# Kernel tuning notes

Measured on AMD Instinct MI355X. Metric: run time of the kernel, lower is better.

The kernel has to match this reference:

```python
import jax, jax.numpy as jnp
import numpy as np

N, E, D, H = 50000, 400000, 64, 2  # nodes, edges, model_dim, heads


def setup_inputs() -> dict:
    key = jax.random.key(0)
    ks = jax.random.split(key, 11)
    lim = 1.0 / np.sqrt(D)        # torch Linear default init bound (fan_in = D)
    lim_o = 1.0 / np.sqrt(H * D)  # O has fan_in = H*D under merge='cat'
    u = lambda k, shape, l: jax.random.uniform(k, shape, jnp.float32, -l, l)
    return {
        "node_feature": jax.random.normal(ks[0], (N, D), jnp.float32),
        "Wk": u(ks[1], (H, D, D), lim), "bk": u(ks[2], (H, D), lim),
        "Wq": u(ks[3], (H, D, D), lim), "bq": u(ks[4], (H, D), lim),
        "Wv": u(ks[5], (H, D, D), lim), "bv": u(ks[6], (H, D), lim),
        "Wo": u(ks[7], (D, H * D), lim_o), "bo": u(ks[8], (D,), lim_o),
        "src": jax.random.randint(ks[9], (E,), 0, N, jnp.int32),
        "dst": jax.random.randint(ks[10], (E,), 0, N, jnp.int32),
    }


def reference(node_feature, Wk, bk, Wq, bq, Wv, bv, Wo, bo, src, dst):
    # message_func: per-edge gather + per-head K/Q/V linears (torch Linear: x @ W.T + b)
    src_nf = node_feature[src]                               # [E, D]
    dst_nf = node_feature[dst]                               # [E, D]
    k = jnp.einsum('ed,hfd->ehf', src_nf, Wk) + bk           # [E, H, D]
    q = jnp.einsum('ed,hfd->ehf', dst_nf, Wq) + bq           # [E, H, D]
    v = jnp.einsum('ed,hfd->ehf', src_nf, Wv) + bv           # [E, H, D]
    score = jnp.sum(k * q, axis=-1)                          # [E, H]

    # reduce_func: mailbox softmax over incoming edges per dst node (segment softmax)
    m = jax.ops.segment_max(score, dst, num_segments=N)      # [N, H]
    m = jnp.where(jnp.isfinite(m), m, jnp.zeros_like(m))     # nodes with no in-edges
    es = jnp.exp(score - m[dst])                             # [E, H]
    denom = jax.ops.segment_sum(es, dst, num_segments=N)     # [N, H]
    w = es / denom[dst]                                      # [E, H] attention weights
    wv = jax.ops.segment_sum(w[..., None] * v, dst, num_segments=N)  # [N, H, D]

    # apply_nodes: merge='cat' over heads, then O linear; weight = mean over heads
    out_nf = jnp.einsum('nf,of->no', wv.reshape(N, H * D), Wo) + bo  # [N, D]
    edge_weight = w.mean(axis=-1)                            # [E] (per-edge, mean over heads)
    return out_nf, edge_weight
```

## Files before the change

kernel.cpp:

```cpp
#include <hip/hip_runtime.h>
#include <hip/hip_bf16.h>
#include <cstdint>


#define BCAP 32

using short8 = __attribute__((ext_vector_type(8))) short;
using f32x4 = __attribute__((ext_vector_type(4))) float;

__device__ __forceinline__ unsigned short f2bf(float f) {
  __hip_bfloat16 h = __float2bfloat16(f);
  return *reinterpret_cast<unsigned short*>(&h);
}
__device__ __forceinline__ void bf8(const uint4 u, float* f) {
  union { unsigned int i; float v; } a;
  a.i = u.x << 16; f[0] = a.v;  a.i = u.x & 0xffff0000u; f[1] = a.v;
  a.i = u.y << 16; f[2] = a.v;  a.i = u.y & 0xffff0000u; f[3] = a.v;
  a.i = u.z << 16; f[4] = a.v;  a.i = u.z & 0xffff0000u; f[5] = a.v;
  a.i = u.w << 16; f[6] = a.v;  a.i = u.w & 0xffff0000u; f[7] = a.v;
}
__device__ __forceinline__ float dot8(const uint4 a, const uint4 b, float s) {
  float af[8], bfv[8];
  bf8(a, af);
  bf8(b, bfv);
#pragma unroll
  for (int j = 0; j < 8; ++j) s += af[j] * bfv[j];
  return s;
}
__device__ __forceinline__ float gmax16(float v) {
#pragma unroll
  for (int m = 1; m < 16; m <<= 1) v = fmaxf(v, __shfl_xor(v, m, 64));
  return v;
}
__device__ __forceinline__ float gsum16(float v) {
#pragma unroll
  for (int m = 1; m < 16; m <<= 1) v += __shfl_xor(v, m, 64);
  return v;
}

__global__ __launch_bounds__(256) void prep_kernel(
    const float* __restrict__ nf, unsigned short* __restrict__ nfb,
    const float* __restrict__ Wk, const float* __restrict__ Wq,
    const float* __restrict__ Wv, const float* __restrict__ Wo,
    const float* __restrict__ bq, const float* __restrict__ bv,
    const float* __restrict__ bo,
    unsigned short* __restrict__ Mb, unsigned short* __restrict__ Fb,
    float* __restrict__ qb, float* __restrict__ fbias,
    const int* __restrict__ src, const int* __restrict__ dst,
    int* __restrict__ cnt, int2* __restrict__ bucket,
    int nf_f4, int E, int SB, int FB) {
  if (blockIdx.x < SB) {
    for (int idx = blockIdx.x * 256 + threadIdx.x; idx < 16576; idx += SB * 256) {
      if (idx < 8192) {
        const int hf = idx >> 6, j = idx & 63, h = hf >> 6, f = hf & 63;
        const float* wkp = Wk + h * 4096 + f;
        const float* wqp = Wq + h * 4096 + j;
        float s = 0.f;
        for (int i = 0; i < 64; ++i) s += wkp[i * 64] * wqp[i * 64];
        Mb[idx] = f2bf(s);
      } else if (idx < 16384) {
        const int r = idx - 8192;
        const int o = r >> 7, hj = r & 127, h = hj >> 6, j = hj & 63;
        const float* wop = Wo + o * 128 + h * 64;
        const float* wvp = Wv + h * 4096 + j;
        float s = 0.f;
        for (int i = 0; i < 64; ++i) s += wop[i] * wvp[i * 64];
        Fb[r] = f2bf(s);
      } else if (idx < 16512) {
        const int hf = idx - 16384, h = hf >> 6, f = hf & 63;
        const float* wkp = Wk + h * 4096 + f;
        const float* bqp = bq + h * 64;
        float s = 0.f;
        for (int i = 0; i < 64; ++i) s += wkp[i * 64] * bqp[i];
        qb[hf] = s;
      } else if (idx < 16576) {
        const int o = idx - 16512;
        float s = bo[o];
        for (int hi = 0; hi < 128; ++hi) s += Wo[o * 128 + hi] * bv[hi];
        fbias[o] = s;
      }
    }
    return;
  }
  if (blockIdx.x < SB + FB) {
    for (int i = (blockIdx.x - SB) * 256 + threadIdx.x; i < nf_f4; i += FB * 256) {
      const float4 x = ((const float4*)nf)[i];
      uint2 p;
      p.x = (unsigned)f2bf(x.x) | ((unsigned)f2bf(x.y) << 16);
      p.y = (unsigned)f2bf(x.z) | ((unsigned)f2bf(x.w) << 16);
      ((uint2*)nfb)[i] = p;
    }
    return;
  }
  const int CB = gridDim.x - SB - FB;
  for (int e = (blockIdx.x - SB - FB) * 256 + threadIdx.x; e < E; e += CB * 256) {
    const int d = dst[e];
    const int pos = atomicAdd(&cnt[d], 1);
    if (pos < BCAP) bucket[(size_t)d * BCAP + pos] = make_int2(e, src[e]);
  }
}

__global__ __launch_bounds__(256) void qt_kernel(
    const unsigned short* __restrict__ nfb, const unsigned short* __restrict__ Mb,
    const float* __restrict__ qb, unsigned short* __restrict__ Qtb, int N) {
  const int lane = threadIdx.x & 63;
  const int wid = threadIdx.x >> 6;
  const int base = (blockIdx.x * 4 + wid) * 32;
  if (base >= N) return;
  const int col = lane & 15;
  const int kslot = lane >> 4;
  const int k0 = kslot * 8;

  short8 fb[2][2];
#pragma unroll
  for (int t = 0; t < 2; ++t) {
    const int node = min(base + t * 16 + col, N - 1);
    const unsigned short* np = nfb + (size_t)node * 64;
    fb[t][0] = *(const short8*)(np + k0);
    fb[t][1] = *(const short8*)(np + 32 + k0);
  }

#pragma unroll
  for (int t8 = 0; t8 < 8; ++t8) {
    const unsigned short* mp = Mb + (size_t)(t8 * 16 + col) * 64;
    const short8 fa0 = *(const short8*)(mp + k0);
    const short8 fa1 = *(const short8*)(mp + 32 + k0);
    const int wf = t8 * 16 + kslot * 4;
    const float4 bias = *(const float4*)(qb + wf);
#pragma unroll
    for (int t = 0; t < 2; ++t) {
      f32x4 acc = {0.f, 0.f, 0.f, 0.f};
      acc = __builtin_amdgcn_mfma_f32_16x16x32_bf16(fa0, fb[t][0], acc, 0, 0, 0);
      acc = __builtin_amdgcn_mfma_f32_16x16x32_bf16(fa1, fb[t][1], acc, 0, 0, 0);
      const int node = base + t * 16 + col;
      if (node < N) {
        uint2 p;
        p.x = (unsigned)f2bf(acc[0] + bias.x) | ((unsigned)f2bf(acc[1] + bias.y) << 16);
        p.y = (unsigned)f2bf(acc[2] + bias.z) | ((unsigned)f2bf(acc[3] + bias.w) << 16);
        *(uint2*)(Qtb + (size_t)node * 128 + wf) = p;
      }
    }
  }
}

__global__ __launch_bounds__(256) void node_kernel(
    const unsigned short* __restrict__ nfb, const unsigned short* __restrict__ Qtb,
    const int2* __restrict__ bucket, const int* __restrict__ cnt,
    const unsigned short* __restrict__ Fb, const float* __restrict__ fbias,
    const float* __restrict__ bo,
    float* __restrict__ out, float* __restrict__ eout, int N) {
  __shared__ uint4 swv[16][16];

  const int lane = threadIdx.x & 63;
  const int wid = threadIdx.x >> 6;
  const int sl = lane & 15;
  const int g16 = lane & 48;
  const int c8 = sl & 7;
  const int nl = wid * 4 + (lane >> 4);
  const int node = blockIdx.x * 16 + nl;
  const bool valid = node < N;
  const int nodeq = valid ? node : N - 1;
  const int deg = valid ? min(cnt[node], BCAP) : 0;

  int wdeg = deg;
  wdeg = max(wdeg, __shfl_xor(wdeg, 16, 64));
  wdeg = max(wdeg, __shfl_xor(wdeg, 32, 64));
  wdeg = __builtin_amdgcn_readfirstlane(wdeg);

  const uint4 qt = ((const uint4*)(Qtb + (size_t)nodeq * 128))[sl];

  uint4 packed = make_uint4(0u, 0u, 0u, 0u);

  if (wdeg <= 16) {
    int2 es = make_int2(0, 0);
    if (sl < deg) es = bucket[(size_t)nodeq * BCAP + sl];
    const int e_my = es.x;
    const int s_my = (sl < deg) ? es.y : 0;

    int s_i[16];
#pragma unroll
    for (int i = 0; i < 16; ++i) s_i[i] = __shfl(s_my, g16 + i, 64);

    uint4 x_i[16];
#pragma unroll
    for (int i = 0; i < 16; ++i)
      x_i[i] = *(const uint4*)(nfb + (size_t)s_i[i] * 64 + c8 * 8);

    float sc0 = -1e30f, sc1 = -1e30f;
#pragma unroll
    for (int i = 0; i < 16; ++i) {
      float p = dot8(x_i[i], qt, 0.f);
#pragma unroll
      for (int m = 1; m < 8; m <<= 1) p += __shfl_xor(p, m, 64);
      const float other = __shfl_xor(p, 8, 64);
      const float t0 = (sl < 8) ? p : other;
      const float t1 = (sl < 8) ? other : p;
      if (sl == i) { sc0 = t0; sc1 = t1; }
    }
    if (sl >= deg) { sc0 = -1e30f; sc1 = -1e30f; }

    const float m0 = gmax16(sc0);
    const float m1 = gmax16(sc1);
    const float w0 = __expf(sc0 - m0);
    const float w1 = __expf(sc1 - m1);
    const float den0 = gsum16(w0);
    const float den1 = gsum16(w1);
    if (sl < deg) eout[e_my] = 0.5f * (w0 / den0 + w1 / den1);

    float agg[8];
#pragma unroll
    for (int j = 0; j < 8; ++j) agg[j] = 0.f;
#pragma unroll
    for (int i = 0; i < 16; ++i) {
      const float wi0 = __shfl(w0, g16 + i, 64);
      const float wi1 = __shfl(w1, g16 + i, 64);
      float xf[8];
      bf8(x_i[i], xf);
      const float ws = (sl < 8) ? wi0 : wi1;
#pragma unroll
      for (int j = 0; j < 8; ++j) agg[j] += ws * xf[j];
    }
    const float dinv = (deg == 0) ? 0.f : ((sl < 8) ? 1.f / den0 : 1.f / den1);
    unsigned short ob[8];
#pragma unroll
    for (int j = 0; j < 8; ++j) ob[j] = f2bf(agg[j] * dinv);
    packed = *(const uint4*)ob;
  } else {
    float m0 = -1e30f, m1 = -1e30f, den0 = 0.f, den1 = 0.f;
    float agg[8];
#pragma unroll
    for (int j = 0; j < 8; ++j) agg[j] = 0.f;

    for (int c0 = 0; c0 < deg; c0 += 16) {
      const int cn = min(16, deg - c0);
      int s_my = 0;
      if (sl < cn) s_my = bucket[(size_t)nodeq * BCAP + c0 + sl].y;

      int s_i[16];
#pragma unroll
      for (int i = 0; i < 16; ++i) s_i[i] = __shfl(s_my, g16 + i, 64);
      uint4 x_i[16];
#pragma unroll
      for (int i = 0; i < 16; ++i)
        x_i[i] = *(const uint4*)(nfb + (size_t)s_i[i] * 64 + c8 * 8);

      float sc0 = -1e30f, sc1 = -1e30f;
#pragma unroll
      for (int i = 0; i < 16; ++i) {
        float p = dot8(x_i[i], qt, 0.f);
#pragma unroll
        for (int m = 1; m < 8; m <<= 1) p += __shfl_xor(p, m, 64);
        const float other = __shfl_xor(p, 8, 64);
        const float t0 = (sl < 8) ? p : other;
        const float t1 = (sl < 8) ? other : p;
        if (sl == i) { sc0 = t0; sc1 = t1; }
      }
      if (sl >= cn) { sc0 = -1e30f; sc1 = -1e30f; }

      const float cm0 = gmax16(sc0);
      const float cm1 = gmax16(sc1);
      const float nm0 = fmaxf(m0, cm0), nm1 = fmaxf(m1, cm1);
      const float r0 = __expf(m0 - nm0), r1 = __expf(m1 - nm1);
      den0 *= r0; den1 *= r1;
      const float racc = (sl < 8) ? r0 : r1;
#pragma unroll
      for (int j = 0; j < 8; ++j) agg[j] *= racc;
      m0 = nm0; m1 = nm1;

      const float w0 = __expf(sc0 - m0);
      const float w1 = __expf(sc1 - m1);
      den0 += gsum16(w0);
      den1 += gsum16(w1);

#pragma unroll
      for (int i = 0; i < 16; ++i) {
        const float wi0 = __shfl(w0, g16 + i, 64);
        const float wi1 = __shfl(w1, g16 + i, 64);
        float xf[8];
        bf8(x_i[i], xf);
        const float ws = (sl < 8) ? wi0 : wi1;
#pragma unroll
        for (int j = 0; j < 8; ++j) agg[j] += ws * xf[j];
      }
    }

    const float dinv = (deg == 0) ? 0.f : ((sl < 8) ? 1.f / den0 : 1.f / den1);
    unsigned short ob[8];
#pragma unroll
    for (int j = 0; j < 8; ++j) ob[j] = f2bf(agg[j] * dinv);
    packed = *(const uint4*)ob;

    for (int i = 0; i < deg; ++i) {
      const int2 es = bucket[(size_t)nodeq * BCAP + i];
      const uint4 xv = *(const uint4*)(nfb + (size_t)es.y * 64 + c8 * 8);
      float p = dot8(xv, qt, 0.f);
#pragma unroll
      for (int m = 1; m < 8; m <<= 1) p += __shfl_xor(p, m, 64);
      const float other = __shfl_xor(p, 8, 64);
      const float t0 = (sl < 8) ? p : other;
      const float t1 = (sl < 8) ? other : p;
      if (sl == 0)
        eout[es.x] = 0.5f * (__expf(t0 - m0) / den0 + __expf(t1 - m1) / den1);
    }
  }

  swv[nl][sl ^ nl] = packed;
  __syncthreads();

  const int col16 = lane & 15;
  const int hi = lane >> 4;
  short8 fa[4];
#pragma unroll
  for (int c = 0; c < 4; ++c)
    fa[c] = *(const short8*)&swv[col16][(c * 4 + hi) ^ col16];

  const int o = wid * 16 + col16;
  const unsigned short* bp = Fb + (size_t)o * 128;
  f32x4 acco = {0.f, 0.f, 0.f, 0.f};
#pragma unroll
  for (int c = 0; c < 4; ++c) {
    const short8 fbb = *(const short8*)(bp + c * 32 + hi * 8);
    acco = __builtin_amdgcn_mfma_f32_16x16x32_bf16(fa[c], fbb, acco, 0, 0, 0);
  }
  const float fb_o = fbias[o];
  const float bo_o = bo[o];
#pragma unroll
  for (int r = 0; r < 4; ++r) {
    const int nrow = blockIdx.x * 16 + hi * 4 + r;
    if (nrow < N) {
      const float bias = (cnt[nrow] > 0) ? fb_o : bo_o;
      out[(size_t)nrow * 64 + o] = acco[r] + bias;
    }
  }
}

extern "C" void kernel_launch(void* const* d_in, const int* in_sizes, int n_in,
                              void* d_out, int out_size, void* d_ws, size_t ws_size,
                              hipStream_t stream) {
  const float* nf = (const float*)d_in[0];
  const float* Wk = (const float*)d_in[1];
  const float* Wq = (const float*)d_in[3];
  const float* bq = (const float*)d_in[4];
  const float* Wv = (const float*)d_in[5];
  const float* bv = (const float*)d_in[6];
  const float* Wo = (const float*)d_in[7];
  const float* bo = (const float*)d_in[8];
  const int* src = (const int*)d_in[9];
  const int* dst = (const int*)d_in[10];

  const int N = in_sizes[0] / 64;
  const int E = in_sizes[9];

  float* out_nf = (float*)d_out;
  float* eout = (float*)d_out + (size_t)N * 64;

  char* w = (char*)d_ws;
  auto alloc = [&](size_t bytes) -> void* {
    void* p = (void*)w;
    w += (bytes + 255) / 256 * 256;
    return p;
  };
  unsigned short* nfb = (unsigned short*)alloc((size_t)N * 64 * 2);
  unsigned short* Qtb = (unsigned short*)alloc((size_t)N * 128 * 2);
  unsigned short* Mb = (unsigned short*)alloc((size_t)128 * 64 * 2);
  unsigned short* Fb = (unsigned short*)alloc((size_t)64 * 128 * 2);
  float* qb = (float*)alloc(128 * 4);
  float* fbias = (float*)alloc(64 * 4);
  int* cnt = (int*)alloc((size_t)N * 4);
  int2* bucket = (int2*)alloc((size_t)N * BCAP * 8);

  const int SB = 16;
  const int FB = 128;
  const int CB = 256;
  const int nf_f4 = (N * 64) / 4;

  hipMemsetAsync(cnt, 0, (size_t)N * 4, stream);

  prep_kernel<<<SB + FB + CB, 256, 0, stream>>>(
      nf, nfb, Wk, Wq, Wv, Wo, bq, bv, bo, Mb, Fb, qb, fbias, src, dst, cnt,
      bucket, nf_f4, E, SB, FB);
  qt_kernel<<<(N + 127) / 128, 256, 0, stream>>>(nfb, Mb, qb, Qtb, N);
  node_kernel<<<(N + 15) / 16, 256, 0, stream>>>(nfb, Qtb, bucket, cnt, Fb,
                                                 fbias, bo, out_nf, eout, N);
}
```

Measured before the change: 103.9 us.

## Fuse per-node Q-transform MFMA into node kernel via shared memory

Removes the separate qt_kernel and computes each block's 16 nodes' transformed query vectors inside node_kernel with MFMA, storing them in a swizzled shared-memory tile instead of a global Qtb buffer. This eliminates one kernel launch and the global write and read of an N x 128 bf16 intermediate. In exchange it adds a __syncthreads, extra shared memory and a reload of the Mb weights per block, which may lower occupancy slightly.

```diff
diff --git a/kernel.cpp b/kernel.cpp
--- a/kernel.cpp
+++ b/kernel.cpp
@@ -100,64 +100,54 @@
   }
 }
 
-__global__ __launch_bounds__(256) void qt_kernel(
-    const unsigned short* __restrict__ nfb, const unsigned short* __restrict__ Mb,
-    const float* __restrict__ qb, unsigned short* __restrict__ Qtb, int N) {
-  const int lane = threadIdx.x & 63;
-  const int wid = threadIdx.x >> 6;
-  const int base = (blockIdx.x * 4 + wid) * 32;
-  if (base >= N) return;
-  const int col = lane & 15;
-  const int kslot = lane >> 4;
-  const int k0 = kslot * 8;
-
-  short8 fb[2][2];
-#pragma unroll
-  for (int t = 0; t < 2; ++t) {
-    const int node = min(base + t * 16 + col, N - 1);
-    const unsigned short* np = nfb + (size_t)node * 64;
-    fb[t][0] = *(const short8*)(np + k0);
-    fb[t][1] = *(const short8*)(np + 32 + k0);
-  }
-
-#pragma unroll
-  for (int t8 = 0; t8 < 8; ++t8) {
-    const unsigned short* mp = Mb + (size_t)(t8 * 16 + col) * 64;
-    const short8 fa0 = *(const short8*)(mp + k0);
-    const short8 fa1 = *(const short8*)(mp + 32 + k0);
-    const int wf = t8 * 16 + kslot * 4;
-    const float4 bias = *(const float4*)(qb + wf);
-#pragma unroll
-    for (int t = 0; t < 2; ++t) {
-      f32x4 acc = {0.f, 0.f, 0.f, 0.f};
-      acc = __builtin_amdgcn_mfma_f32_16x16x32_bf16(fa0, fb[t][0], acc, 0, 0, 0);
-      acc = __builtin_amdgcn_mfma_f32_16x16x32_bf16(fa1, fb[t][1], acc, 0, 0, 0);
-      const int node = base + t * 16 + col;
-      if (node < N) {
-        uint2 p;
-        p.x = (unsigned)f2bf(acc[0] + bias.x) | ((unsigned)f2bf(acc[1] + bias.y) << 16);
-        p.y = (unsigned)f2bf(acc[2] + bias.z) | ((unsigned)f2bf(acc[3] + bias.w) << 16);
-        *(uint2*)(Qtb + (size_t)node * 128 + wf) = p;
-      }
-    }
-  }
-}
-
 __global__ __launch_bounds__(256) void node_kernel(
-    const unsigned short* __restrict__ nfb, const unsigned short* __restrict__ Qtb,
+    const unsigned short* __restrict__ nfb,
+    const unsigned short* __restrict__ Mb, const float* __restrict__ qb,
     const int2* __restrict__ bucket, const int* __restrict__ cnt,
     const unsigned short* __restrict__ Fb, const float* __restrict__ fbias,
     const float* __restrict__ bo,
     float* __restrict__ out, float* __restrict__ eout, int N) {
+  __shared__ uint4 sqt[16][16];
   __shared__ uint4 swv[16][16];
 
   const int lane = threadIdx.x & 63;
   const int wid = threadIdx.x >> 6;
+  const int col = lane & 15;
+  const int kslot = lane >> 4;
+  const int k0 = kslot * 8;
+  const int base = blockIdx.x * 16;
+
+  {
+    const int bnode = min(base + col, N - 1);
+    const unsigned short* np = nfb + (size_t)bnode * 64;
+    const short8 xb0 = *(const short8*)(np + k0);
+    const short8 xb1 = *(const short8*)(np + 32 + k0);
+#pragma unroll
+    for (int tt = 0; tt < 2; ++tt) {
+      const int t8 = wid * 2 + tt;
+      const unsigned short* mp = Mb + (size_t)(t8 * 16 + col) * 64;
+      const short8 fa0 = *(const short8*)(mp + k0);
+      const short8 fa1 = *(const short8*)(mp + 32 + k0);
+      f32x4 acc = {0.f, 0.f, 0.f, 0.f};
+      acc = __builtin_amdgcn_mfma_f32_16x16x32_bf16(fa0, xb0, acc, 0, 0, 0);
+      acc = __builtin_amdgcn_mfma_f32_16x16x32_bf16(fa1, xb1, acc, 0, 0, 0);
+      const int hf = t8 * 16 + kslot * 4;
+      const float4 bias = *(const float4*)(qb + hf);
+      uint2 p;
+      p.x = (unsigned)f2bf(acc[0] + bias.x) | ((unsigned)f2bf(acc[1] + bias.y) << 16);
+      p.y = (unsigned)f2bf(acc[2] + bias.z) | ((unsigned)f2bf(acc[3] + bias.w) << 16);
+      const int c4 = hf >> 3;
+      const int sub = (hf >> 2) & 1;
+      ((uint2*)&sqt[col][c4 ^ col])[sub] = p;
+    }
+  }
+  __syncthreads();
+
   const int sl = lane & 15;
   const int g16 = lane & 48;
   const int c8 = sl & 7;
   const int nl = wid * 4 + (lane >> 4);
-  const int node = blockIdx.x * 16 + nl;
+  const int node = base + nl;
   const bool valid = node < N;
   const int nodeq = valid ? node : N - 1;
   const int deg = valid ? min(cnt[node], BCAP) : 0;
@@ -167,7 +157,7 @@
   wdeg = max(wdeg, __shfl_xor(wdeg, 32, 64));
   wdeg = __builtin_amdgcn_readfirstlane(wdeg);
 
-  const uint4 qt = ((const uint4*)(Qtb + (size_t)nodeq * 128))[sl];
+  const uint4 qt = sqt[nl][sl ^ nl];
 
   uint4 packed = make_uint4(0u, 0u, 0u, 0u);
 
@@ -307,14 +297,13 @@
   swv[nl][sl ^ nl] = packed;
   __syncthreads();
 
-  const int col16 = lane & 15;
   const int hi = lane >> 4;
   short8 fa[4];
 #pragma unroll
   for (int c = 0; c < 4; ++c)
-    fa[c] = *(const short8*)&swv[col16][(c * 4 + hi) ^ col16];
-
-  const int o = wid * 16 + col16;
+    fa[c] = *(const short8*)&swv[col][(c * 4 + hi) ^ col];
+
+  const int o = wid * 16 + col;
   const unsigned short* bp = Fb + (size_t)o * 128;
   f32x4 acco = {0.f, 0.f, 0.f, 0.f};
 #pragma unroll
@@ -326,7 +315,7 @@
   const float bo_o = bo[o];
 #pragma unroll
   for (int r = 0; r < 4; ++r) {
-    const int nrow = blockIdx.x * 16 + hi * 4 + r;
+    const int nrow = base + hi * 4 + r;
     if (nrow < N) {
       const float bias = (cnt[nrow] > 0) ? fb_o : bo_o;
       out[(size_t)nrow * 64 + o] = acco[r] + bias;
@@ -361,7 +350,6 @@
     return p;
   };
   unsigned short* nfb = (unsigned short*)alloc((size_t)N * 64 * 2);
-  unsigned short* Qtb = (unsigned short*)alloc((size_t)N * 128 * 2);
   unsigned short* Mb = (unsigned short*)alloc((size_t)128 * 64 * 2);
   unsigned short* Fb = (unsigned short*)alloc((size_t)64 * 128 * 2);
   float* qb = (float*)alloc(128 * 4);
@@ -379,7 +367,6 @@
   prep_kernel<<<SB + FB + CB, 256, 0, stream>>>(
       nf, nfb, Wk, Wq, Wv, Wo, bq, bv, bo, Mb, Fb, qb, fbias, src, dst, cnt,
       bucket, nf_f4, E, SB, FB);
-  qt_kernel<<<(N + 127) / 128, 256, 0, stream>>>(nfb, Mb, qb, Qtb, N);
-  node_kernel<<<(N + 15) / 16, 256, 0, stream>>>(nfb, Qtb, bucket, cnt, Fb,
+  node_kernel<<<(N + 15) / 16, 256, 0, stream>>>(nfb, Mb, qb, bucket, cnt, Fb,
                                                  fbias, bo, out_nf, eout, N);
 }
```

Result: faster. 98.94 us (-4.8%).
